# Performance work log

Hardware: AMD Instinct MI355X
Metric: run time of the kernel (lower is better)

The kernel has to match this reference:

```python
import jax, jax.numpy as jnp
import numpy as np

B, N, C = 8, 4096, 768
H = 8            # num_heads (hardcoded in module)
D = C // H       # head_dim = 96


def setup_inputs() -> dict:
    key = jax.random.key(0)
    ks = jax.random.split(key, 10)
    s = 0.02
    return {
        "x_rgb": jax.random.normal(ks[0], (B, N, C), dtype=jnp.float32),
        "x_depth": jax.random.normal(ks[1], (B, N, C), dtype=jnp.float32),
        "W_qkv_rgb": jax.random.normal(ks[2], (3 * C, C), dtype=jnp.float32) * s,
        "b_qkv_rgb": jnp.zeros((3 * C,), dtype=jnp.float32),
        "W_qkv_depth": jax.random.normal(ks[3], (2 * C, C), dtype=jnp.float32) * s,
        "b_qkv_depth": jnp.zeros((2 * C,), dtype=jnp.float32),
        "W_out": jax.random.normal(ks[4], (C, C), dtype=jnp.float32) * s,
        "b_out": jnp.zeros((C,), dtype=jnp.float32),
        "adaptive_weights": jnp.ones((2,), dtype=jnp.float32),
    }


def reference(x_rgb, x_depth, W_qkv_rgb, b_qkv_rgb, W_qkv_depth, b_qkv_depth,
              W_out, b_out, adaptive_weights):
    scale = 1.0 / (D ** 0.5)
    # qkv projections (torch Linear: x @ W.T + b)
    qkv_rgb = (x_rgb @ W_qkv_rgb.T + b_qkv_rgb).reshape(B, N, 3, H, D)
    q_rgb, k_rgb, v_rgb = qkv_rgb[:, :, 0], qkv_rgb[:, :, 1], qkv_rgb[:, :, 2]
    kv_depth = (x_depth @ W_qkv_depth.T + b_qkv_depth).reshape(B, N, 2, H, D)
    k_depth, v_depth = kv_depth[:, :, 0], kv_depth[:, :, 1]

    # per-token attention across the head axis: scores are [B,N,H,H]
    attn_rgb = jax.nn.softmax(
        jnp.einsum('bnqd,bnkd->bnqk', q_rgb, k_depth) * scale, axis=-1)
    attn_depth = jax.nn.softmax(
        jnp.einsum('bnqd,bnkd->bnqk', q_rgb, k_rgb) * scale, axis=-1)

    # NOTE: faithful to original einsum with independent labels k and v:
    # sums over k (softmax -> 1) and over v independently.
    wv_rgb = jnp.einsum('bnqk,bnvd->bnqd', attn_rgb, v_depth)
    wv_depth = jnp.einsum('bnqk,bnvd->bnqd', attn_depth, v_rgb)

    w = jax.nn.sigmoid(adaptive_weights)
    x_fusion = (w[0] * wv_rgb + w[1] * wv_depth).reshape(B, N, C)
    x_fusion = x_fusion @ W_out.T + b_out
    return (x_rgb, x_fusion)
```

## Files before the change

kernel.cpp:

```cpp
#include <hip/hip_runtime.h>

typedef unsigned short u16;
typedef __attribute__((ext_vector_type(8))) short bf16x8;
typedef __attribute__((ext_vector_type(4))) float f32x4;

#define M_TOT 32768

__device__ __forceinline__ u16 f2b(float x) {
    union { float f; unsigned u; } c; c.f = x;
    unsigned r = c.u + 0x7fffu + ((c.u >> 16) & 1u);
    return (u16)(r >> 16);
}

__global__ void prep_b1(const float* __restrict__ Wr, const float* __restrict__ Wd,
                        const float* __restrict__ br, const float* __restrict__ bd,
                        const float* __restrict__ aw,
                        u16* __restrict__ B1, float* __restrict__ fb) {
    int id = blockIdx.x * 256 + threadIdx.x;
    if (id >= 96 * 1536) return;
    int d = id / 1536, k = id - d * 1536;
    float w0 = 1.f / (1.f + __expf(-aw[0]));
    float w1 = 1.f / (1.f + __expf(-aw[1]));
    float s = 0.f, v;
    if (k < 768) {
        for (int h = 0; h < 8; h++) s += Wr[(size_t)(1536 + h * 96 + d) * 768 + k];
        v = w1 * s;
    } else {
        for (int h = 0; h < 8; h++) s += Wd[(size_t)(768 + h * 96 + d) * 768 + (k - 768)];
        v = w0 * s;
    }
    B1[id] = f2b(v);
    if (k == 0) {
        float t = 0.f;
        for (int h = 0; h < 8; h++)
            t += w1 * br[1536 + h * 96 + d] + w0 * bd[768 + h * 96 + d];
        fb[d] = t;
    }
}

__global__ void prep_weff(const float* __restrict__ Wo, u16* __restrict__ Weff) {
    int id = blockIdx.x * 256 + threadIdx.x;
    if (id >= 768 * 96) return;
    int c = id / 96, d = id - c * 96;
    float s = 0.f;
    for (int h = 0; h < 8; h++) s += Wo[(size_t)c * 768 + h * 96 + d];
    Weff[id] = f2b(s);
}

#define LDF 72
__global__ __launch_bounds__(256) void gemm_f(const float* __restrict__ Xr,
                                              const float* __restrict__ Xd,
                                              const u16* __restrict__ B1,
                                              const float* __restrict__ fb,
                                              float* __restrict__ out0,
                                              u16* __restrict__ fbuf) {
    __shared__ u16 sA[64 * LDF];
    __shared__ u16 sB[96 * LDF];
    const int tid = threadIdx.x;
    const int m0 = blockIdx.x * 64;
    const int lane = tid & 63, wave = tid >> 6;
    const int fr = lane & 15, fk = (lane >> 4) * 8;

    f32x4 acc[6] = {};

    for (int ks = 0; ks < 24; ks++) {
        const int k0 = ks * 64;
        const float* __restrict__ X = (ks < 12) ? Xr : Xd;
        const int kx = (ks < 12) ? k0 : (k0 - 768);

#pragma unroll
        for (int r = 0; r < 4; r++) {
            int c = tid + 256 * r;
            int row = c >> 4, colc = (c & 15) * 4;
            float4 v = *(const float4*)&X[(size_t)(m0 + row) * 768 + kx + colc];
            if (ks < 12)
                *(float4*)&out0[(size_t)(m0 + row) * 768 + k0 + colc] = v;
            ushort4 bv;
            bv.x = f2b(v.x); bv.y = f2b(v.y); bv.z = f2b(v.z); bv.w = f2b(v.w);
            *(ushort4*)&sA[row * LDF + colc] = bv;
        }
#pragma unroll
        for (int r = 0; r < 3; r++) {
            int c = tid + 256 * r;
            int row = c >> 3, colc = (c & 7) * 8;
            *(uint4*)&sB[row * LDF + colc] =
                *(const uint4*)&B1[(size_t)row * 1536 + k0 + colc];
        }
        __syncthreads();

#pragma unroll
        for (int s = 0; s < 2; s++) {
            bf16x8 a = *(bf16x8*)&sA[(wave * 16 + fr) * LDF + s * 32 + fk];
#pragma unroll
            for (int j = 0; j < 6; j++) {
                bf16x8 b = *(bf16x8*)&sB[(j * 16 + fr) * LDF + s * 32 + fk];
                acc[j] = __builtin_amdgcn_mfma_f32_16x16x32_bf16(a, b, acc[j], 0, 0, 0);
            }
        }
        __syncthreads();
    }

    const int em = (lane >> 4) * 4, en = lane & 15;
#pragma unroll
    for (int j = 0; j < 6; j++) {
        int dcol = j * 16 + en;
        float bias = fb[dcol];
#pragma unroll
        for (int r = 0; r < 4; r++) {
            int row = m0 + wave * 16 + em + r;
            fbuf[(size_t)row * 96 + dcol] = f2b(acc[j][r] + bias);
        }
    }
}

#define LDO 104
__global__ __launch_bounds__(256) void gemm_o(const u16* __restrict__ fbuf,
                                              const u16* __restrict__ Weff,
                                              const float* __restrict__ bout,
                                              float* __restrict__ out1) {
    __shared__ u16 sA[128 * LDO];
    __shared__ u16 sB[128 * LDO];
    const int tid = threadIdx.x;
    const int n0 = blockIdx.x * 128, m0 = blockIdx.y * 128;

#pragma unroll
    for (int r = 0; r < 6; r++) {
        int c = tid + 256 * r;
        int row = c / 12, colc = (c - row * 12) * 8;
        *(uint4*)&sA[row * LDO + colc] =
            *(const uint4*)&fbuf[(size_t)(m0 + row) * 96 + colc];
        *(uint4*)&sB[row * LDO + colc] =
            *(const uint4*)&Weff[(size_t)(n0 + row) * 96 + colc];
    }
    __syncthreads();

    const int lane = tid & 63, wave = tid >> 6;
    const int wm = (wave >> 1) * 64, wn = (wave & 1) * 64;
    const int fr = lane & 15, fk = (lane >> 4) * 8;

    f32x4 acc[4][4] = {};
#pragma unroll
    for (int s = 0; s < 3; s++) {
        bf16x8 a[4], b[4];
#pragma unroll
        for (int i = 0; i < 4; i++)
            a[i] = *(bf16x8*)&sA[(wm + i * 16 + fr) * LDO + s * 32 + fk];
#pragma unroll
        for (int j = 0; j < 4; j++)
            b[j] = *(bf16x8*)&sB[(wn + j * 16 + fr) * LDO + s * 32 + fk];
#pragma unroll
        for (int i = 0; i < 4; i++)
#pragma unroll
            for (int j = 0; j < 4; j++)
                acc[i][j] = __builtin_amdgcn_mfma_f32_16x16x32_bf16(a[i], b[j], acc[i][j], 0, 0, 0);
    }

    const int em = (lane >> 4) * 4, en = lane & 15;
#pragma unroll
    for (int j = 0; j < 4; j++) {
        int col = n0 + wn + j * 16 + en;
        float bias = bout[col];
#pragma unroll
        for (int i = 0; i < 4; i++) {
#pragma unroll
            for (int r = 0; r < 4; r++) {
                out1[(size_t)(m0 + wm + i * 16 + em + r) * 768 + col] = acc[i][j][r] + bias;
            }
        }
    }
}

extern "C" void kernel_launch(void* const* d_in, const int* in_sizes, int n_in,
                              void* d_out, int out_size, void* d_ws, size_t ws_size,
                              hipStream_t stream) {
    const float* x_rgb       = (const float*)d_in[0];
    const float* x_depth     = (const float*)d_in[1];
    const float* W_qkv_rgb   = (const float*)d_in[2];
    const float* b_qkv_rgb   = (const float*)d_in[3];
    const float* W_qkv_depth = (const float*)d_in[4];
    const float* b_qkv_depth = (const float*)d_in[5];
    const float* W_out       = (const float*)d_in[6];
    const float* b_out       = (const float*)d_in[7];
    const float* aw          = (const float*)d_in[8];

    float* out0 = (float*)d_out;
    float* out1 = out0 + (size_t)M_TOT * 768;

    char* w = (char*)d_ws;
    u16*   B1   = (u16*)w;
    float* fb   = (float*)(w + 294912);
    u16*   Weff = (u16*)(w + 294912 + 512);
    u16*   fbuf = (u16*)(w + 294912 + 512 + 147456);

    prep_b1<<<576, 256, 0, stream>>>(W_qkv_rgb, W_qkv_depth, b_qkv_rgb, b_qkv_depth,
                                     aw, B1, fb);
    prep_weff<<<288, 256, 0, stream>>>(W_out, Weff);
    gemm_f<<<512, 256, 0, stream>>>(x_rgb, x_depth, B1, fb, out0, fbuf);
    gemm_o<<<dim3(6, 256), 256, 0, stream>>>(fbuf, Weff, b_out, out1);
}
```

Measured before the change: 405.3 us.

## Drop LDS staging in both GEMMs; load MFMA fragments directly from global

Both GEMM kernels stop staging tiles in shared memory and removing barriers. Each wave instead loads its MFMA operand fragments straight from global memory. gemm_f gains register prefetch of the next K-step's activations, and gemm_o switches to a 16x96 tile per wave with a 1D grid of 4096 blocks. This is meant to cut LDS traffic and synchronization in what is a memory-bound workload. The trade-off is that B fragments are re-read from global or L2 by every wave, and the stores are less coalesced.

```diff
diff --git a/kernel.cpp b/kernel.cpp
--- a/kernel.cpp
+++ b/kernel.cpp
@@ -47,126 +47,121 @@
     Weff[id] = f2b(s);
 }
 
-#define LDF 72
 __global__ __launch_bounds__(256) void gemm_f(const float* __restrict__ Xr,
                                               const float* __restrict__ Xd,
                                               const u16* __restrict__ B1,
                                               const float* __restrict__ fb,
                                               float* __restrict__ out0,
                                               u16* __restrict__ fbuf) {
-    __shared__ u16 sA[64 * LDF];
-    __shared__ u16 sB[96 * LDF];
     const int tid = threadIdx.x;
-    const int m0 = blockIdx.x * 64;
-    const int lane = tid & 63, wave = tid >> 6;
-    const int fr = lane & 15, fk = (lane >> 4) * 8;
+    const int lane = tid & 63;
+    const int wv = (blockIdx.x << 2) | (tid >> 6);
+    const int fr = lane & 15;
+    const int fk = (lane >> 4) << 3;
+    const size_t arow = (size_t)((wv << 4) | fr) * 768 + fk;
+
+    const float* __restrict__ pr = Xr + arow;
+    const float* __restrict__ pd = Xd + arow;
+    float* __restrict__ po = out0 + arow;
+    const u16* __restrict__ pb = B1 + fr * 1536 + fk;
 
     f32x4 acc[6] = {};
 
+    float4 a0 = *(const float4*)(pr);
+    float4 a1 = *(const float4*)(pr + 4);
+    float4 a2 = *(const float4*)(pr + 32);
+    float4 a3 = *(const float4*)(pr + 36);
+
     for (int ks = 0; ks < 24; ks++) {
         const int k0 = ks * 64;
-        const float* __restrict__ X = (ks < 12) ? Xr : Xd;
-        const int kx = (ks < 12) ? k0 : (k0 - 768);
 
+        const float* pn = (ks >= 23) ? pr
+                        : ((ks + 1 < 12) ? (pr + k0 + 64) : (pd + k0 - 704));
+        float4 n0 = *(const float4*)(pn);
+        float4 n1 = *(const float4*)(pn + 4);
+        float4 n2 = *(const float4*)(pn + 32);
+        float4 n3 = *(const float4*)(pn + 36);
+
+        if (ks < 12) {
+            *(float4*)(po + k0)      = a0;
+            *(float4*)(po + k0 + 4)  = a1;
+            *(float4*)(po + k0 + 32) = a2;
+            *(float4*)(po + k0 + 36) = a3;
+        }
+
+        bf16x8 ab0, ab1;
+        ab0[0] = (short)f2b(a0.x); ab0[1] = (short)f2b(a0.y);
+        ab0[2] = (short)f2b(a0.z); ab0[3] = (short)f2b(a0.w);
+        ab0[4] = (short)f2b(a1.x); ab0[5] = (short)f2b(a1.y);
+        ab0[6] = (short)f2b(a1.z); ab0[7] = (short)f2b(a1.w);
+        ab1[0] = (short)f2b(a2.x); ab1[1] = (short)f2b(a2.y);
+        ab1[2] = (short)f2b(a2.z); ab1[3] = (short)f2b(a2.w);
+        ab1[4] = (short)f2b(a3.x); ab1[5] = (short)f2b(a3.y);
+        ab1[6] = (short)f2b(a3.z); ab1[7] = (short)f2b(a3.w);
+
+        const u16* pbk = pb + k0;
 #pragma unroll
-        for (int r = 0; r < 4; r++) {
-            int c = tid + 256 * r;
-            int row = c >> 4, colc = (c & 15) * 4;
-            float4 v = *(const float4*)&X[(size_t)(m0 + row) * 768 + kx + colc];
-            if (ks < 12)
-                *(float4*)&out0[(size_t)(m0 + row) * 768 + k0 + colc] = v;
-            ushort4 bv;
-            bv.x = f2b(v.x); bv.y = f2b(v.y); bv.z = f2b(v.z); bv.w = f2b(v.w);
-            *(ushort4*)&sA[row * LDF + colc] = bv;
-        }
+        for (int j = 0; j < 6; j++)
+            acc[j] = __builtin_amdgcn_mfma_f32_16x16x32_bf16(
+                ab0, *(const bf16x8*)(pbk + j * 24576), acc[j], 0, 0, 0);
 #pragma unroll
-        for (int r = 0; r < 3; r++) {
-            int c = tid + 256 * r;
-            int row = c >> 3, colc = (c & 7) * 8;
-            *(uint4*)&sB[row * LDF + colc] =
-                *(const uint4*)&B1[(size_t)row * 1536 + k0 + colc];
-        }
-        __syncthreads();
+        for (int j = 0; j < 6; j++)
+            acc[j] = __builtin_amdgcn_mfma_f32_16x16x32_bf16(
+                ab1, *(const bf16x8*)(pbk + j * 24576 + 32), acc[j], 0, 0, 0);
 
-#pragma unroll
-        for (int s = 0; s < 2; s++) {
-            bf16x8 a = *(bf16x8*)&sA[(wave * 16 + fr) * LDF + s * 32 + fk];
-#pragma unroll
-            for (int j = 0; j < 6; j++) {
-                bf16x8 b = *(bf16x8*)&sB[(j * 16 + fr) * LDF + s * 32 + fk];
-                acc[j] = __builtin_amdgcn_mfma_f32_16x16x32_bf16(a, b, acc[j], 0, 0, 0);
-            }
-        }
-        __syncthreads();
+        a0 = n0; a1 = n1; a2 = n2; a3 = n3;
     }
 
-    const int em = (lane >> 4) * 4, en = lane & 15;
+    const int em = (lane >> 4) << 2, en = lane & 15;
+    const int orow = (wv << 4) + em;
 #pragma unroll
     for (int j = 0; j < 6; j++) {
-        int dcol = j * 16 + en;
-        float bias = fb[dcol];
+        const int dcol = j * 16 + en;
+        const float bias = fb[dcol];
 #pragma unroll
-        for (int r = 0; r < 4; r++) {
-            int row = m0 + wave * 16 + em + r;
-            fbuf[(size_t)row * 96 + dcol] = f2b(acc[j][r] + bias);
-        }
+        for (int r = 0; r < 4; r++)
+            fbuf[(size_t)(orow + r) * 96 + dcol] = f2b(acc[j][r] + bias);
     }
 }
 
-#define LDO 104
 __global__ __launch_bounds__(256) void gemm_o(const u16* __restrict__ fbuf,
                                               const u16* __restrict__ Weff,
                                               const float* __restrict__ bout,
                                               float* __restrict__ out1) {
-    __shared__ u16 sA[128 * LDO];
-    __shared__ u16 sB[128 * LDO];
     const int tid = threadIdx.x;
-    const int n0 = blockIdx.x * 128, m0 = blockIdx.y * 128;
+    const int lane = tid & 63;
+    const int wv = (blockIdx.x << 2) | (tid >> 6);
+    const int mg = wv >> 3;
+    const int nc = (wv & 7) * 96;
+    const int fr = lane & 15, fk = (lane >> 4) << 3;
 
+    const u16* pa = fbuf + (size_t)((mg << 4) | fr) * 96 + fk;
+    bf16x8 A0 = *(const bf16x8*)(pa);
+    bf16x8 A1 = *(const bf16x8*)(pa + 32);
+    bf16x8 A2 = *(const bf16x8*)(pa + 64);
+
+    const u16* pb = Weff + (size_t)(nc + fr) * 96 + fk;
+    f32x4 acc[6] = {};
 #pragma unroll
-    for (int r = 0; r < 6; r++) {
-        int c = tid + 256 * r;
-        int row = c / 12, colc = (c - row * 12) * 8;
-        *(uint4*)&sA[row * LDO + colc] =
-            *(const uint4*)&fbuf[(size_t)(m0 + row) * 96 + colc];
-        *(uint4*)&sB[row * LDO + colc] =
-            *(const uint4*)&Weff[(size_t)(n0 + row) * 96 + colc];
-    }
-    __syncthreads();
-
-    const int lane = tid & 63, wave = tid >> 6;
-    const int wm = (wave >> 1) * 64, wn = (wave & 1) * 64;
-    const int fr = lane & 15, fk = (lane >> 4) * 8;
-
-    f32x4 acc[4][4] = {};
-#pragma unroll
-    for (int s = 0; s < 3; s++) {
-        bf16x8 a[4], b[4];
-#pragma unroll
-        for (int i = 0; i < 4; i++)
-            a[i] = *(bf16x8*)&sA[(wm + i * 16 + fr) * LDO + s * 32 + fk];
-#pragma unroll
-        for (int j = 0; j < 4; j++)
-            b[j] = *(bf16x8*)&sB[(wn + j * 16 + fr) * LDO + s * 32 + fk];
-#pragma unroll
-        for (int i = 0; i < 4; i++)
-#pragma unroll
-            for (int j = 0; j < 4; j++)
-                acc[i][j] = __builtin_amdgcn_mfma_f32_16x16x32_bf16(a[i], b[j], acc[i][j], 0, 0, 0);
+    for (int j = 0; j < 6; j++) {
+        const u16* pbj = pb + j * 1536;
+        acc[j] = __builtin_amdgcn_mfma_f32_16x16x32_bf16(
+            A0, *(const bf16x8*)(pbj), acc[j], 0, 0, 0);
+        acc[j] = __builtin_amdgcn_mfma_f32_16x16x32_bf16(
+            A1, *(const bf16x8*)(pbj + 32), acc[j], 0, 0, 0);
+        acc[j] = __builtin_amdgcn_mfma_f32_16x16x32_bf16(
+            A2, *(const bf16x8*)(pbj + 64), acc[j], 0, 0, 0);
     }
 
-    const int em = (lane >> 4) * 4, en = lane & 15;
+    const int em = (lane >> 4) << 2, en = lane & 15;
+    const int orow = (mg << 4) + em;
 #pragma unroll
-    for (int j = 0; j < 4; j++) {
-        int col = n0 + wn + j * 16 + en;
-        float bias = bout[col];
+    for (int j = 0; j < 6; j++) {
+        const int col = nc + j * 16 + en;
+        const float bias = bout[col];
 #pragma unroll
-        for (int i = 0; i < 4; i++) {
-#pragma unroll
-            for (int r = 0; r < 4; r++) {
-                out1[(size_t)(m0 + wm + i * 16 + em + r) * 768 + col] = acc[i][j][r] + bias;
-            }
-        }
+        for (int r = 0; r < 4; r++)
+            out1[(size_t)(orow + r) * 768 + col] = acc[j][r] + bias;
     }
 }
 
@@ -196,5 +191,5 @@
                                      aw, B1, fb);
     prep_weff<<<288, 256, 0, stream>>>(W_out, Weff);
     gemm_f<<<512, 256, 0, stream>>>(x_rgb, x_depth, B1, fb, out0, fbuf);
-    gemm_o<<<dim3(6, 256), 256, 0, stream>>>(fbuf, Weff, b_out, out1);
+    gemm_o<<<4096, 256, 0, stream>>>(fbuf, Weff, b_out, out1);
 }
```

After: 443.6 us. +9.5%, slower.
